# Optimization experiments

Hardware: AMD Instinct MI355X
Metric: run time of the kernel (lower is better)

## Reference

```python
import jax, jax.numpy as jnp
import numpy as np

B, S, D = 4, 2048, 1024
H, HD = 16, 64
DFF = 4096
EPS = 1e-6


def setup_inputs() -> dict:
    key = jax.random.key(0)
    ks = jax.random.split(key, 16)
    sc = 0.02
    def w(k, shape):
        return jax.random.normal(k, shape, dtype=jnp.float32) * sc
    return {
        'x': jax.random.normal(ks[0], (B, S, D), dtype=jnp.float32),
        'wq': w(ks[1], (D, D)), 'bq': jnp.zeros((D,), jnp.float32),
        'wk': w(ks[2], (D, D)), 'bk': jnp.zeros((D,), jnp.float32),
        'wv': w(ks[3], (D, D)), 'bv': jnp.zeros((D,), jnp.float32),
        'wo': w(ks[4], (D, D)), 'bo': jnp.zeros((D,), jnp.float32),
        'w1': w(ks[5], (D, DFF)), 'b1': jnp.zeros((DFF,), jnp.float32),
        'w2': w(ks[6], (DFF, D)), 'b2': jnp.zeros((D,), jnp.float32),
        'ln1_a': jnp.ones((D,), jnp.float32), 'ln1_b': jnp.zeros((D,), jnp.float32),
        'ln2_a': jnp.ones((D,), jnp.float32), 'ln2_b': jnp.zeros((D,), jnp.float32),
    }


def layernorm(x, alpha, bias):
    # Matches torch module: std is unbiased (ddof=1), divide by (std + eps)
    mean = jnp.mean(x, axis=-1, keepdims=True)
    var = jnp.sum((x - mean) ** 2, axis=-1, keepdims=True) / (x.shape[-1] - 1)
    std = jnp.sqrt(var)
    return alpha * ((x - mean) / (std + EPS)) + bias


def mha(x, wq, bq, wk, bk, wv, bv, wo, bo):
    q = (x @ wq + bq).reshape(B, S, H, HD)
    k = (x @ wk + bk).reshape(B, S, H, HD)
    v = (x @ wv + bv).reshape(B, S, H, HD)
    scores = jnp.einsum('bqhd,bkhd->bhqk', q, k) / jnp.sqrt(jnp.float32(HD))
    attn = jax.nn.softmax(scores, axis=-1)
    out = jnp.einsum('bhqk,bkhd->bqhd', attn, v).reshape(B, S, D)
    return out @ wo + bo


def reference(x, wq, bq, wk, bk, wv, bv, wo, bo, w1, b1, w2, b2,
              ln1_a, ln1_b, ln2_a, ln2_b):
    # Residual 1: x + MHA(LN(x))   (dropout = identity, eval mode)
    x = x + mha(layernorm(x, ln1_a, ln1_b), wq, bq, wk, bk, wv, bv, wo, bo)
    # Residual 2: x + FFN(LN(x))
    h = layernorm(x, ln2_a, ln2_b)
    ffn = jax.nn.relu(h @ w1 + b1) @ w2 + b2
    return x + ffn
```

## Files before the change

kernel.cpp:

```cpp
#include <hip/hip_runtime.h>

#define S_ 2048
#define D_ 1024

typedef unsigned short u16;
typedef unsigned int u32;
typedef __bf16 bf16x8 __attribute__((ext_vector_type(8)));
typedef unsigned short us8 __attribute__((ext_vector_type(8)));
typedef unsigned short us4 __attribute__((ext_vector_type(4)));
typedef unsigned int u32x4 __attribute__((ext_vector_type(4)));
typedef float f32x4 __attribute__((ext_vector_type(4)));

#if __has_builtin(__builtin_amdgcn_exp2f)
#define EXP2(x) __builtin_amdgcn_exp2f(x)
#else
#define EXP2(x) exp2f(x)
#endif

static __device__ __forceinline__ u16 f2bf(float f) {
  unsigned u = __builtin_bit_cast(unsigned, f);
  u += 0x7fffu + ((u >> 16) & 1u);
  return (u16)(u >> 16);
}

static __device__ __forceinline__ unsigned cvtpk_bf16(float lo, float hi) {
  unsigned r;
  asm("v_cvt_pk_bf16_f32 %0, %1, %2" : "=v"(r) : "v"(lo), "v"(hi));
  return r;
}

static __device__ __forceinline__ f32x4 mfma16(bf16x8 a, bf16x8 b, f32x4 c) {
  return __builtin_amdgcn_mfma_f32_16x16x32_bf16(a, b, c, 0, 0, 0);
}

static __device__ __forceinline__ void gload16(const void* g, void* lds) {
  __builtin_amdgcn_global_load_lds((const __attribute__((address_space(1))) void*)g,
                                   (__attribute__((address_space(3))) void*)lds, 16, 0, 0);
}

__global__ __launch_bounds__(256) void wtrans_kernel(const float* __restrict__ in,
                                                     u16* __restrict__ out, int K, int N,
                                                     float scale) {
  __shared__ float t[32][33];
  const int n0 = blockIdx.x * 32, k0 = blockIdx.y * 32;
  const int tx = threadIdx.x, ty = threadIdx.y;
#pragma unroll
  for (int i = 0; i < 4; i++)
    t[ty + 8 * i][tx] = in[(size_t)(k0 + ty + 8 * i) * N + n0 + tx];
  __syncthreads();
#pragma unroll
  for (int i = 0; i < 4; i++)
    out[(size_t)(n0 + ty + 8 * i) * K + k0 + tx] = f2bf(t[tx][ty + 8 * i] * scale);
}

__global__ __launch_bounds__(256) void bcat_kernel(const float* __restrict__ bq,
                                                   const float* __restrict__ bk,
                                                   const float* __restrict__ bv,
                                                   float* __restrict__ out, float qs) {
  const int i = blockIdx.x * 256 + threadIdx.x;
  out[i] = (i < 1024) ? bq[i] * qs : ((i < 2048) ? bk[i - 1024] : bv[i - 2048]);
}

__global__ __launch_bounds__(256) void ln_kernel(const float* __restrict__ in,
                                                 u16* __restrict__ out,
                                                 const float* __restrict__ alpha,
                                                 const float* __restrict__ beta) {
  const int row = blockIdx.x;
  const int tid = threadIdx.x;
  const float4 v = *(const float4*)(in + (size_t)row * D_ + tid * 4);
  float s = v.x + v.y + v.z + v.w;
  float ss = v.x * v.x + v.y * v.y + v.z * v.z + v.w * v.w;
#pragma unroll
  for (int off = 32; off >= 1; off >>= 1) {
    s += __shfl_xor(s, off);
    ss += __shfl_xor(ss, off);
  }
  __shared__ float red[8];
  const int w = tid >> 6, lane = tid & 63;
  if (lane == 0) { red[w] = s; red[4 + w] = ss; }
  __syncthreads();
  s = red[0] + red[1] + red[2] + red[3];
  ss = red[4] + red[5] + red[6] + red[7];
  const float mean = s * (1.0f / D_);
  const float var = (ss - s * mean) * (1.0f / (D_ - 1));
  const float inv = 1.0f / (sqrtf(var) + 1e-6f);
  const int j = tid * 4;
  const float4 av = *(const float4*)(alpha + j);
  const float4 bv = *(const float4*)(beta + j);
  us4 o;
  o[0] = f2bf((v.x - mean) * inv * av.x + bv.x);
  o[1] = f2bf((v.y - mean) * inv * av.y + bv.y);
  o[2] = f2bf((v.z - mean) * inv * av.z + bv.z);
  o[3] = f2bf((v.w - mean) * inv * av.w + bv.w);
  *(us4*)(out + (size_t)row * D_ + j) = o;
}

template <int OM, bool RELU, bool RESID>
__global__ __launch_bounds__(512, 2) void gemm_bt(const u16* __restrict__ A,
                                                  const u16* __restrict__ Bt,
                                                  const float* __restrict__ bias,
                                                  const float* __restrict__ resid,
                                                  void* __restrict__ outp,
                                                  void* __restrict__ out1,
                                                  void* __restrict__ out2, int N, int K) {
  __shared__ u16 lds[3 * 24576];
  const int tid = threadIdx.x;
  const int lane = tid & 63, w = tid >> 6;
  const int g = lane >> 4, r = lane & 15;
  const int wr = w >> 1, wc = w & 1;

  const int gx = gridDim.x;
  const int nwg = gx * gridDim.y;
  const int orig = blockIdx.y * gx + blockIdx.x;
  const int nid = (orig & 7) * (nwg >> 3) + (orig >> 3);
  const int bx = nid % gx, by = nid / gx;
  const size_t row0 = (size_t)by * 256;
  const int col0 = bx * 128;

  float bias4[4];
#pragma unroll
  for (int n = 0; n < 4; n++) bias4[n] = bias[col0 + wc * 64 + n * 16 + r];

  f32x4 acc[4][4];
#pragma unroll
  for (int m = 0; m < 4; m++)
#pragma unroll
    for (int n = 0; n < 4; n++) {
      f32x4 z = {bias4[n], bias4[n], bias4[n], bias4[n]};
      acc[m][n] = z;
    }

  const int lrow = w * 8 + (lane >> 3);
  const int scol = 8 * ((lane & 7) ^ (lane >> 3));
  const u16* gA = A + (row0 + lrow) * (size_t)K + scol;
  const u16* gB = Bt + ((size_t)col0 + lrow) * (size_t)K + scol;
  const int nt = K >> 6;
  const int sw = (r & 7) << 3;

  int bufi = 0;
#pragma unroll
  for (int t0 = 0; t0 < 2; t0++) {
    u16* dA = lds + t0 * 24576 + w * 512;
#pragma unroll
    for (int j = 0; j < 4; j++) gload16(gA + (size_t)(j * 64) * K + t0 * 64, dA + j * 4096);
#pragma unroll
    for (int j = 0; j < 2; j++)
      gload16(gB + (size_t)(j * 64) * K + t0 * 64, dA + 16384 + j * 4096);
  }

  for (int t = 0; t < nt; ++t) {
    if (t + 1 < nt)
      asm volatile("s_waitcnt vmcnt(6)" ::: "memory");
    else
      asm volatile("s_waitcnt vmcnt(0)" ::: "memory");
    __builtin_amdgcn_s_barrier();
    asm volatile("" ::: "memory");
    const bool st = (t + 2 < nt);
    const int bn = (bufi + 2 >= 3) ? bufi - 1 : bufi + 2;
    u16* dS = lds + bn * 24576 + w * 512;
    const size_t ko = (size_t)(t + 2) * 64;
    const u16* As_ = lds + bufi * 24576;
    const u16* Bs_ = As_ + 16384;
    bf16x8 bfr[2][4];

#pragma unroll
    for (int p = 0; p < 4; ++p) {
      bf16x8 a0 = __builtin_bit_cast(
          bf16x8, *(const us8*)(As_ + (wr * 64 + p * 16 + r) * 64 + ((g * 8) ^ sw)));
      bf16x8 a1 = __builtin_bit_cast(
          bf16x8, *(const us8*)(As_ + (wr * 64 + p * 16 + r) * 64 + ((32 + g * 8) ^ sw)));
      if (p == 0) {
#pragma unroll
        for (int kk = 0; kk < 2; kk++)
#pragma unroll
          for (int n = 0; n < 4; n++)
            bfr[kk][n] = __builtin_bit_cast(
                bf16x8,
                *(const us8*)(Bs_ + (wc * 64 + n * 16 + r) * 64 + ((kk * 32 + g * 8) ^ sw)));
      }
      if (st) {
        if (p == 0) {
          gload16(gA + ko, dS);
          gload16(gA + (size_t)64 * K + ko, dS + 4096);
        } else if (p == 1) {
          gload16(gA + (size_t)128 * K + ko, dS + 8192);
          gload16(gA + (size_t)192 * K + ko, dS + 12288);
        } else if (p == 2) {
          gload16(gB + ko, dS + 16384);
          gload16(gB + (size_t)64 * K + ko, dS + 20480);
        }
      }
      asm volatile("s_waitcnt lgkmcnt(0)" ::: "memory");
      __builtin_amdgcn_sched_barrier(0);
      __builtin_amdgcn_s_setprio(1);
#pragma unroll
      for (int n = 0; n < 4; n++) {
        acc[p][n] = mfma16(a0, bfr[0][n], acc[p][n]);
        acc[p][n] = mfma16(a1, bfr[1][n], acc[p][n]);
      }
      __builtin_amdgcn_s_setprio(0);
      if (p < 3) __builtin_amdgcn_s_barrier();
    }
    bufi = (bufi == 2) ? 0 : bufi + 1;
  }

#pragma unroll
  for (int m = 0; m < 4; m++)
#pragma unroll
    for (int n = 0; n < 4; n++) {
      if (OM == 2) {
        const int seg = col0 >> 10;
        const int cl = (col0 & 1023) + wc * 64 + n * 16 + r;
        if (seg == 2) {
          const int head = cl >> 6, hd = cl & 63;
          const size_t rg0 = row0 + wr * 64 + m * 16 + 4 * g;
          const int b = (int)(rg0 >> 11), s0 = (int)(rg0 & 2047);
          us4 o;
#pragma unroll
          for (int i = 0; i < 4; i++) o[i] = f2bf(acc[m][n][i]);
          *(us4*)((u16*)out2 + (((size_t)(b * 16 + head) * 64 + hd) * S_ + s0)) = o;
        } else {
          u16* dst = (u16*)(seg == 0 ? outp : out1);
#pragma unroll
          for (int i = 0; i < 4; i++) {
            const size_t rg = row0 + wr * 64 + m * 16 + 4 * g + i;
            dst[rg * D_ + cl] = f2bf(acc[m][n][i]);
          }
        }
      } else {
#pragma unroll
        for (int i = 0; i < 4; i++) {
          const size_t rg = row0 + wr * 64 + m * 16 + 4 * g + i;
          const int cg = col0 + wc * 64 + n * 16 + r;
          float v = acc[m][n][i];
          if (RESID) v += resid[rg * N + cg];
          if (RELU) v = fmaxf(v, 0.0f);
          if (OM == 1)
            ((float*)outp)[rg * N + cg] = v;
          else
            ((u16*)outp)[rg * N + cg] = f2bf(v);
        }
      }
    }
}

__global__ __launch_bounds__(256) void attn_kernel(const u16* __restrict__ Q,
                                                   const u16* __restrict__ Km,
                                                   const u16* __restrict__ Vt_g,
                                                   u16* __restrict__ O) {
  __shared__ u16 Klds[64 * 64];
  __shared__ u16 Vlds[64 * 68];
  const int tid = threadIdx.x;
  const int lane = tid & 63, w = tid >> 6;
  const int g = lane >> 4, r = lane & 15;
  const int bh = blockIdx.y;
  const int b = bh >> 4, head = bh & 15;
  const size_t rowbase = (size_t)b * S_;
  const int colbase = head * 64;
  const int qw = blockIdx.x * 128 + w * 32;

  bf16x8 qf0[2], qf1[2];
#pragma unroll
  for (int qh = 0; qh < 2; qh++) {
    const u16* qrow = Q + (rowbase + qw + qh * 16 + r) * D_ + colbase;
    qf0[qh] = __builtin_bit_cast(bf16x8, *(const us8*)(qrow + g * 8));
    qf1[qh] = __builtin_bit_cast(bf16x8, *(const us8*)(qrow + 32 + g * 8));
  }

  const int srow = tid >> 3;
  const int sslot = (tid & 7) ^ (srow & 7);
  const u16* Kg = Km + (rowbase + srow) * D_ + colbase + sslot * 8;
  const u16* Vg = Vt_g + ((size_t)bh * 64 + srow) * S_ + (tid & 7) * 8;
  char* lK = (char*)Klds + w * 1024;

  float l_run[2] = {0.0f, 0.0f};
  f32x4 oacc[2][4];
#pragma unroll
  for (int qh = 0; qh < 2; qh++)
#pragma unroll
    for (int n = 0; n < 4; n++) {
      f32x4 z = {0.0f, 0.0f, 0.0f, 0.0f};
      oacc[qh][n] = z;
    }

  for (int kt = 0; kt < S_ / 64; kt++) {
    const us8 v0 = *(const us8*)(Vg + (size_t)kt * 64);
    const us8 v1 = *(const us8*)(Vg + 32 * S_ + (size_t)kt * 64);
    __syncthreads();
    gload16(Kg + (size_t)kt * 64 * D_, lK);
    gload16(Kg + (size_t)(kt * 64 + 32) * D_, lK + 4096);
    *(us8*)(Vlds + srow * 68 + (tid & 7) * 8) = v0;
    *(us8*)(Vlds + (srow + 32) * 68 + (tid & 7) * 8) = v1;
    __syncthreads();

    f32x4 st[4][2];
    __builtin_amdgcn_s_setprio(1);
#pragma unroll
    for (int f = 0; f < 4; f++) {
      const int row = f * 16 + r;
      const int sw = row & 7;
      const bf16x8 k0 = __builtin_bit_cast(bf16x8, *(const us8*)(Klds + row * 64 + (g ^ sw) * 8));
      const bf16x8 k1 =
          __builtin_bit_cast(bf16x8, *(const us8*)(Klds + row * 64 + ((g + 4) ^ sw) * 8));
#pragma unroll
      for (int qh = 0; qh < 2; qh++) {
        f32x4 z = {0.0f, 0.0f, 0.0f, 0.0f};
        st[f][qh] = mfma16(k0, qf0[qh], z);
        st[f][qh] = mfma16(k1, qf1[qh], st[f][qh]);
      }
    }
    __builtin_amdgcn_s_setprio(0);
    u32 pw[2][8];
#pragma unroll
    for (int qh = 0; qh < 2; qh++)
#pragma unroll
      for (int f = 0; f < 4; f++) {
        const float e0 = EXP2(st[f][qh][0]);
        const float e1 = EXP2(st[f][qh][1]);
        const float e2 = EXP2(st[f][qh][2]);
        const float e3 = EXP2(st[f][qh][3]);
        l_run[qh] += (e0 + e1) + (e2 + e3);
        pw[qh][f * 2] = cvtpk_bf16(e0, e1);
        pw[qh][f * 2 + 1] = cvtpk_bf16(e2, e3);
      }

    bf16x8 a0[2], a1[2];
#pragma unroll
    for (int qh = 0; qh < 2; qh++) {
      const u32x4 a0w = {pw[qh][0], pw[qh][1], pw[qh][2], pw[qh][3]};
      const u32x4 a1w = {pw[qh][4], pw[qh][5], pw[qh][6], pw[qh][7]};
      a0[qh] = __builtin_bit_cast(bf16x8, a0w);
      a1[qh] = __builtin_bit_cast(bf16x8, a1w);
    }
    __builtin_amdgcn_s_setprio(1);
#pragma unroll
    for (int n = 0; n < 4; n++) {
      const u16* vr = Vlds + (n * 16 + r) * 68;
      const us4 v00 = *(const us4*)(vr + g * 4);
      const us4 v01 = *(const us4*)(vr + 16 + g * 4);
      const us4 v10 = *(const us4*)(vr + 32 + g * 4);
      const us4 v11 = *(const us4*)(vr + 48 + g * 4);
      const bf16x8 vb0 =
          __builtin_bit_cast(bf16x8, __builtin_shufflevector(v00, v01, 0, 1, 2, 3, 4, 5, 6, 7));
      const bf16x8 vb1 =
          __builtin_bit_cast(bf16x8, __builtin_shufflevector(v10, v11, 0, 1, 2, 3, 4, 5, 6, 7));
#pragma unroll
      for (int qh = 0; qh < 2; qh++) {
        oacc[qh][n] = mfma16(a0[qh], vb0, oacc[qh][n]);
        oacc[qh][n] = mfma16(a1[qh], vb1, oacc[qh][n]);
      }
    }
    __builtin_amdgcn_s_setprio(0);
  }

#pragma unroll
  for (int qh = 0; qh < 2; qh++) {
    l_run[qh] += __shfl_xor(l_run[qh], 16);
    l_run[qh] += __shfl_xor(l_run[qh], 32);
    float ld[4];
#pragma unroll
    for (int i = 0; i < 4; i++) ld[i] = 1.0f / __shfl(l_run[qh], 4 * g + i);
#pragma unroll
    for (int n = 0; n < 4; n++)
#pragma unroll
      for (int i = 0; i < 4; i++)
        O[(rowbase + qw + qh * 16 + 4 * g + i) * D_ + colbase + n * 16 + r] =
            f2bf(oacc[qh][n][i] * ld[i]);
  }
}

extern "C" void kernel_launch(void* const* d_in, const int* in_sizes, int n_in, void* d_out,
                              int out_size, void* d_ws, size_t ws_size, hipStream_t stream) {
  (void)in_sizes; (void)n_in; (void)out_size; (void)ws_size;
  const float* x = (const float*)d_in[0];
  const float* wq = (const float*)d_in[1];
  const float* bq = (const float*)d_in[2];
  const float* wk = (const float*)d_in[3];
  const float* bk = (const float*)d_in[4];
  const float* wv = (const float*)d_in[5];
  const float* bv = (const float*)d_in[6];
  const float* wo = (const float*)d_in[7];
  const float* bo = (const float*)d_in[8];
  const float* w1 = (const float*)d_in[9];
  const float* b1 = (const float*)d_in[10];
  const float* w2 = (const float*)d_in[11];
  const float* b2 = (const float*)d_in[12];
  const float* ln1a = (const float*)d_in[13];
  const float* ln1b = (const float*)d_in[14];
  const float* ln2a = (const float*)d_in[15];
  const float* ln2b = (const float*)d_in[16];

  char* ws = (char*)d_ws;
  const size_t MB = 1ull << 20;
  u16* wqkv = (u16*)(ws + 0 * MB);
  u16* wqt = wqkv;
  u16* wkt = (u16*)(ws + 2 * MB);
  u16* wvt = (u16*)(ws + 4 * MB);
  u16* wot = (u16*)(ws + 6 * MB);
  u16* w1t = (u16*)(ws + 8 * MB);
  u16* w2t = (u16*)(ws + 16 * MB);
  u16* xA = (u16*)(ws + 24 * MB);
  u16* qb = (u16*)(ws + 40 * MB);
  u16* kb = (u16*)(ws + 56 * MB);
  u16* vt = (u16*)(ws + 72 * MB);
  float* bcat = (float*)(ws + 88 * MB);
  u16* ff1 = (u16*)(ws + 40 * MB);
  float* x1 = (float*)(ws + 104 * MB);

  const float QSCALE = 0.125f * 1.4426950408889634f;

  const dim3 tb(32, 8);
  wtrans_kernel<<<dim3(32, 32), tb, 0, stream>>>(wq, wqt, 1024, 1024, QSCALE);
  wtrans_kernel<<<dim3(32, 32), tb, 0, stream>>>(wk, wkt, 1024, 1024, 1.0f);
  wtrans_kernel<<<dim3(32, 32), tb, 0, stream>>>(wv, wvt, 1024, 1024, 1.0f);
  wtrans_kernel<<<dim3(32, 32), tb, 0, stream>>>(wo, wot, 1024, 1024, 1.0f);
  wtrans_kernel<<<dim3(128, 32), tb, 0, stream>>>(w1, w1t, 1024, 4096, 1.0f);
  wtrans_kernel<<<dim3(32, 128), tb, 0, stream>>>(w2, w2t, 4096, 1024, 1.0f);
  bcat_kernel<<<12, 256, 0, stream>>>(bq, bk, bv, bcat, QSCALE);

  ln_kernel<<<8192, 256, 0, stream>>>(x, xA, ln1a, ln1b);
  gemm_bt<2, false, false><<<dim3(24, 32), 512, 0, stream>>>(xA, wqkv, bcat, nullptr, qb, kb, vt,
                                                             3072, 1024);
  attn_kernel<<<dim3(16, 64), 256, 0, stream>>>(qb, kb, vt, xA);
  gemm_bt<1, false, true><<<dim3(8, 32), 512, 0, stream>>>(xA, wot, bo, x, x1, nullptr, nullptr,
                                                           1024, 1024);
  ln_kernel<<<8192, 256, 0, stream>>>(x1, xA, ln2a, ln2b);
  gemm_bt<0, true, false><<<dim3(32, 32), 512, 0, stream>>>(xA, w1t, b1, nullptr, ff1, nullptr,
                                                            nullptr, 4096, 1024);
  gemm_bt<1, false, true><<<dim3(8, 32), 512, 0, stream>>>(ff1, w2t, b2, x1, (float*)d_out,
                                                           nullptr, nullptr, 1024, 4096);
}
```

Measured before the change: 394.5 us.

## Add 256x256-tile GEMM for FFN1 and compute softmax row sums via MFMA

Adds a new GEMM kernel with 256x256 output tiles, double-buffered LDS loaded via direct global-to-LDS loads, XCD-aware block remapping and bias folded into the accumulator init. It replaces the 128-tile FFN up-projection and is meant to raise arithmetic intensity and cut global traffic. Separately, the attention kernel now computes the softmax denominator with an MFMA against a ones vector instead of scalar adds plus cross-lane shuffles, taking VALU work off the inner loop. The large tile needs 128 KB LDS and many accumulator registers, which limits occupancy. Summing the bf16-rounded probabilities also makes the denominator match the numerator's rounding.

```diff
diff --git a/kernel.cpp b/kernel.cpp
--- a/kernel.cpp
+++ b/kernel.cpp
@@ -244,6 +244,119 @@
     }
 }
 
+template <bool RELU>
+__global__ __launch_bounds__(512, 2) void gemm_bt256(const u16* __restrict__ A,
+                                                     const u16* __restrict__ Bt,
+                                                     const float* __restrict__ bias,
+                                                     u16* __restrict__ outp, int N, int K) {
+  __shared__ u16 lds[2 * 32768];
+  const int tid = threadIdx.x;
+  const int lane = tid & 63, w = tid >> 6;
+  const int g = lane >> 4, r = lane & 15;
+  const int wr = w >> 2, wc = w & 3;
+  const int gx = gridDim.x;
+  const int nwg = gx * gridDim.y;
+  const int orig = blockIdx.y * gx + blockIdx.x;
+  const int nid = (orig & 7) * (nwg >> 3) + (orig >> 3);
+  const int bx = nid % gx, by = nid / gx;
+  const size_t row0 = (size_t)by * 256;
+  const int col0 = bx * 256;
+
+  float bias4[4];
+#pragma unroll
+  for (int n = 0; n < 4; n++) bias4[n] = bias[col0 + wc * 64 + n * 16 + r];
+
+  f32x4 acc[8][4];
+#pragma unroll
+  for (int m = 0; m < 8; m++)
+#pragma unroll
+    for (int n = 0; n < 4; n++) {
+      f32x4 z = {bias4[n], bias4[n], bias4[n], bias4[n]};
+      acc[m][n] = z;
+    }
+
+  const int lrow = tid >> 3;
+  const int scol = 8 * ((tid & 7) ^ (lrow & 7));
+  const u16* gA = A + (row0 + lrow) * (size_t)K + scol;
+  const u16* gB = Bt + ((size_t)col0 + lrow) * (size_t)K + scol;
+  const int nt = K >> 6;
+  const int sw = (r & 7) << 3;
+
+  {
+    u16* d = lds + w * 512;
+#pragma unroll
+    for (int j = 0; j < 4; j++) gload16(gA + (size_t)(j * 64) * K, d + j * 4096);
+#pragma unroll
+    for (int j = 0; j < 4; j++) gload16(gB + (size_t)(j * 64) * K, d + 16384 + j * 4096);
+  }
+
+  for (int t = 0; t < nt; ++t) {
+    const u16* As_ = lds + (t & 1) * 32768;
+    const u16* Bs_ = As_ + 16384;
+    if (t + 1 < nt) {
+      u16* d = lds + ((t + 1) & 1) * 32768 + w * 512;
+      const size_t ko = (size_t)(t + 1) * 64;
+#pragma unroll
+      for (int j = 0; j < 4; j++) gload16(gA + (size_t)(j * 64) * K + ko, d + j * 4096);
+#pragma unroll
+      for (int j = 0; j < 4; j++) gload16(gB + (size_t)(j * 64) * K + ko, d + 16384 + j * 4096);
+      asm volatile("s_waitcnt vmcnt(8)" ::: "memory");
+    } else {
+      asm volatile("s_waitcnt vmcnt(0)" ::: "memory");
+    }
+    __builtin_amdgcn_s_barrier();
+    asm volatile("" ::: "memory");
+
+    bf16x8 bfr[2][4];
+#pragma unroll
+    for (int kk = 0; kk < 2; kk++)
+#pragma unroll
+      for (int n = 0; n < 4; n++)
+        bfr[kk][n] = __builtin_bit_cast(
+            bf16x8, *(const us8*)(Bs_ + (wc * 64 + n * 16 + r) * 64 + ((kk * 32 + g * 8) ^ sw)));
+
+#pragma unroll
+    for (int p = 0; p < 4; ++p) {
+      bf16x8 af[2][2];
+#pragma unroll
+      for (int mm = 0; mm < 2; mm++) {
+        const int row = wr * 128 + (p * 2 + mm) * 16 + r;
+        af[0][mm] = __builtin_bit_cast(bf16x8, *(const us8*)(As_ + row * 64 + ((g * 8) ^ sw)));
+        af[1][mm] =
+            __builtin_bit_cast(bf16x8, *(const us8*)(As_ + row * 64 + ((32 + g * 8) ^ sw)));
+      }
+      asm volatile("" ::: "memory");
+      if (p > 0) __builtin_amdgcn_s_barrier();
+      asm volatile("s_waitcnt lgkmcnt(0)" ::: "memory");
+      __builtin_amdgcn_sched_barrier(0);
+      __builtin_amdgcn_s_setprio(1);
+#pragma unroll
+      for (int mm = 0; mm < 2; mm++)
+#pragma unroll
+        for (int n = 0; n < 4; n++) {
+          acc[p * 2 + mm][n] = mfma16(af[0][mm], bfr[0][n], acc[p * 2 + mm][n]);
+          acc[p * 2 + mm][n] = mfma16(af[1][mm], bfr[1][n], acc[p * 2 + mm][n]);
+        }
+      __builtin_amdgcn_s_setprio(0);
+    }
+    asm volatile("" ::: "memory");
+    __builtin_amdgcn_s_barrier();
+  }
+
+#pragma unroll
+  for (int m = 0; m < 8; m++)
+#pragma unroll
+    for (int n = 0; n < 4; n++)
+#pragma unroll
+      for (int i = 0; i < 4; i++) {
+        const size_t rg = row0 + wr * 128 + m * 16 + 4 * g + i;
+        const int cg = col0 + wc * 64 + n * 16 + r;
+        float v = acc[m][n][i];
+        if (RELU) v = fmaxf(v, 0.0f);
+        outp[rg * N + cg] = f2bf(v);
+      }
+}
+
 __global__ __launch_bounds__(256) void attn_kernel(const u16* __restrict__ Q,
                                                    const u16* __restrict__ Km,
                                                    const u16* __restrict__ Vt_g,
@@ -273,15 +386,18 @@
   const u16* Vg = Vt_g + ((size_t)bh * 64 + srow) * S_ + (tid & 7) * 8;
   char* lK = (char*)Klds + w * 1024;
 
-  float l_run[2] = {0.0f, 0.0f};
+  const us8 onesw = {0x3F80, 0x3F80, 0x3F80, 0x3F80, 0x3F80, 0x3F80, 0x3F80, 0x3F80};
+  const bf16x8 ones8 = __builtin_bit_cast(bf16x8, onesw);
+
+  f32x4 lacc[2];
   f32x4 oacc[2][4];
 #pragma unroll
-  for (int qh = 0; qh < 2; qh++)
-#pragma unroll
-    for (int n = 0; n < 4; n++) {
-      f32x4 z = {0.0f, 0.0f, 0.0f, 0.0f};
-      oacc[qh][n] = z;
-    }
+  for (int qh = 0; qh < 2; qh++) {
+    f32x4 z = {0.0f, 0.0f, 0.0f, 0.0f};
+    lacc[qh] = z;
+#pragma unroll
+    for (int n = 0; n < 4; n++) oacc[qh][n] = z;
+  }
 
   for (int kt = 0; kt < S_ / 64; kt++) {
     const us8 v0 = *(const us8*)(Vg + (size_t)kt * 64);
@@ -319,7 +435,6 @@
         const float e1 = EXP2(st[f][qh][1]);
         const float e2 = EXP2(st[f][qh][2]);
         const float e3 = EXP2(st[f][qh][3]);
-        l_run[qh] += (e0 + e1) + (e2 + e3);
         pw[qh][f * 2] = cvtpk_bf16(e0, e1);
         pw[qh][f * 2 + 1] = cvtpk_bf16(e2, e3);
       }
@@ -333,6 +448,11 @@
       a1[qh] = __builtin_bit_cast(bf16x8, a1w);
     }
     __builtin_amdgcn_s_setprio(1);
+#pragma unroll
+    for (int qh = 0; qh < 2; qh++) {
+      lacc[qh] = mfma16(a0[qh], ones8, lacc[qh]);
+      lacc[qh] = mfma16(a1[qh], ones8, lacc[qh]);
+    }
 #pragma unroll
     for (int n = 0; n < 4; n++) {
       const u16* vr = Vlds + (n * 16 + r) * 68;
@@ -355,11 +475,9 @@
 
 #pragma unroll
   for (int qh = 0; qh < 2; qh++) {
-    l_run[qh] += __shfl_xor(l_run[qh], 16);
-    l_run[qh] += __shfl_xor(l_run[qh], 32);
     float ld[4];
 #pragma unroll
-    for (int i = 0; i < 4; i++) ld[i] = 1.0f / __shfl(l_run[qh], 4 * g + i);
+    for (int i = 0; i < 4; i++) ld[i] = 1.0f / lacc[qh][i];
 #pragma unroll
     for (int n = 0; n < 4; n++)
 #pragma unroll
@@ -425,8 +543,7 @@
   gemm_bt<1, false, true><<<dim3(8, 32), 512, 0, stream>>>(xA, wot, bo, x, x1, nullptr, nullptr,
                                                            1024, 1024);
   ln_kernel<<<8192, 256, 0, stream>>>(x1, xA, ln2a, ln2b);
-  gemm_bt<0, true, false><<<dim3(32, 32), 512, 0, stream>>>(xA, w1t, b1, nullptr, ff1, nullptr,
-                                                            nullptr, 4096, 1024);
+  gemm_bt256<true><<<dim3(16, 32), 512, 0, stream>>>(xA, w1t, b1, ff1, 4096, 1024);
   gemm_bt<1, false, true><<<dim3(8, 32), 512, 0, stream>>>(ff1, w2t, b2, x1, (float*)d_out,
                                                            nullptr, nullptr, 1024, 4096);
 }
```

Result: faster. 381.6 us (-3.3%).
